# Performance work log

Hardware: AMD Instinct MI355X
Metric: run time of the kernel (lower is better)

## Reference

```python
import jax, jax.numpy as jnp
import numpy as np

# dims
B, S, H, D = 1, 2048, 32, 128
BLOCK = 64          # sparse_block_size
LOCAL = 16          # local_blocks
VERT = 8            # vert_stride
OFFSET = 0          # head_sliding_offset
SLIDE = max(1, VERT // H)  # head_sliding_step = max(1, int(vert_stride / num_heads))
NEG_INF = -1e30


def _sparse_mask():
    """Token-level local+vertical-stride causal mask, [H, S, S] bool."""
    pos = jnp.arange(S)
    blk = pos // BLOCK                                  # block index per token
    causal = pos[:, None] >= pos[None, :]               # [S, S]
    local = (blk[:, None] - blk[None, :]) < LOCAL       # [S, S]
    h = jnp.arange(H)
    # per-head vertical strips on key blocks
    vert = ((blk[None, None, :] + h[:, None, None] * SLIDE + OFFSET + 1) % VERT) == 0  # [H,1,S]
    return causal[None, :, :] & (local[None, :, :] | vert)  # [H, S, S]


def setup_inputs() -> dict:
    key = jax.random.key(0)
    kq, kk, kv = jax.random.split(key, 3)
    shape = (B, S, H, D)
    return {
        "query": jax.random.normal(kq, shape, dtype=jnp.float32),
        "key": jax.random.normal(kk, shape, dtype=jnp.float32),
        "value": jax.random.normal(kv, shape, dtype=jnp.float32),
    }


def reference(query, key, value):
    # inputs are bshd; sm_scale = head_dim**-0.5 (dkernel default)
    scale = 1.0 / jnp.sqrt(jnp.asarray(D, dtype=query.dtype))
    mask = _sparse_mask()                               # [H, S, S]
    scores = jnp.einsum("bqhd,bkhd->bhqk", query, key) * scale
    scores = jnp.where(mask[None], scores, NEG_INF)
    probs = jax.nn.softmax(scores, axis=-1)
    out = jnp.einsum("bhqk,bkhd->bqhd", probs, value)
    return out
```

## Files before the change

kernel.cpp:

```cpp
#include <hip/hip_runtime.h>


#define NH 32
#define HD 128
#define LOCALB 16

typedef __attribute__((ext_vector_type(8))) short short8;
typedef __attribute__((ext_vector_type(4))) float f32x4;

static __device__ __forceinline__ unsigned f2u(float f) {
    union { float f; unsigned u; } x; x.f = f; return x.u;
}
static __device__ __forceinline__ unsigned bfpk(float a, float b) {
    return ((f2u(a) + 0x8000u) >> 16) | ((f2u(b) + 0x8000u) & 0xFFFF0000u);
}
static __device__ __forceinline__ unsigned short f2bf(float f) {
    return (unsigned short)((f2u(f) + 0x8000u) >> 16);
}

static __device__ __forceinline__ void wg_barrier() {
    asm volatile("" ::: "memory");
    __builtin_amdgcn_s_waitcnt(0xC07F);
    __builtin_amdgcn_s_barrier();
    asm volatile("" ::: "memory");
}

static __device__ __forceinline__ bool blk_active(int qb, int kb, int h) {
    return ((qb - kb) < LOCALB) || (((kb + h + 1) & 7) == 0);
}

static __device__ __forceinline__ int krow(int kk) {
    return (kk & 3) | (((kk >> 2) & 1) << 4) | (((kk >> 3) & 3) << 2) | (kk & 32);
}

__global__ __launch_bounds__(256)
void sparse_attn_kernel(const float* __restrict__ Q,
                        const float* __restrict__ K,
                        const float* __restrict__ V,
                        float* __restrict__ O)
{
    const int id   = blockIdx.x;
    const int h    = (id & 7) * 4 + ((id >> 3) & 3);
    const int qb   = 31 - (id >> 5);

    const int tid  = threadIdx.x;
    const int wave = tid >> 6;
    const int lane = tid & 63;
    const int m16  = lane & 15;
    const int quad = lane >> 4;

    __shared__ __align__(16) char smem[64 * 136 * 2 + 128 * 36 * 4];
    unsigned short (*Ks)[136] = reinterpret_cast<unsigned short(*)[136]>(smem);
    unsigned (*Vp)[36] = reinterpret_cast<unsigned(*)[36]>(smem + 64 * 136 * 2);

    const float QSC = 0.08838834764831845f * 1.44269504088896f;
    short8 qf[4];
    {
        const int qrow = qb * 64 + wave * 16 + m16;
        const float* qp = Q + ((size_t)qrow * NH + h) * HD + quad * 8;
        #pragma unroll
        for (int ks = 0; ks < 4; ++ks) {
            const float4 a = *reinterpret_cast<const float4*>(qp + ks * 32);
            const float4 b = *reinterpret_cast<const float4*>(qp + ks * 32 + 4);
            short8 f;
            f[0]=(short)f2bf(a.x*QSC); f[1]=(short)f2bf(a.y*QSC);
            f[2]=(short)f2bf(a.z*QSC); f[3]=(short)f2bf(a.w*QSC);
            f[4]=(short)f2bf(b.x*QSC); f[5]=(short)f2bf(b.y*QSC);
            f[6]=(short)f2bf(b.z*QSC); f[7]=(short)f2bf(b.w*QSC);
            qf[ks] = f;
        }
    }

    f32x4 acc[8];
    #pragma unroll
    for (int dt = 0; dt < 8; ++dt) { acc[dt][0]=0.f; acc[dt][1]=0.f; acc[dt][2]=0.f; acc[dt][3]=0.f; }
    float mrow = -3.0e38f;
    float lrow = 0.f;

    const int kkey0 = tid >> 5;
    const int kd4   = (tid & 31) << 2;
    const int vkey0 = wave * 8 + (lane & 7);
    const int vd40  = (lane >> 3) << 2;
    const int vc    = wave * 4 + ((lane & 7) >> 1);

    int kb = 0;
    while (!blk_active(qb, kb, h)) ++kb;

    float4 kreg[8], vreg[8];
    {
        const float* kp = K + (size_t)kb * 262144 + (size_t)kkey0 * 4096 + h * 128 + kd4;
        #pragma unroll
        for (int it = 0; it < 8; ++it)
            kreg[it] = *reinterpret_cast<const float4*>(kp + it * 32768);
        const float* vp = V + (size_t)kb * 262144 + (size_t)vkey0 * 4096 + h * 128 + vd40;
        #pragma unroll
        for (int it = 0; it < 8; ++it)
            vreg[it] = *reinterpret_cast<const float4*>(vp + (it & 1) * 131072 + (it >> 1) * 32);
    }

    while (kb <= qb) {
        int nkb = kb + 1;
        while (nkb <= qb && !blk_active(qb, nkb, h)) ++nkb;

        wg_barrier();

        #pragma unroll
        for (int it = 0; it < 8; ++it) {
            const float4 kv = kreg[it];
            uint2 pk; pk.x = bfpk(kv.x, kv.y); pk.y = bfpk(kv.z, kv.w);
            *reinterpret_cast<uint2*>(&Ks[krow(it * 8 + kkey0)][kd4]) = pk;
        }
        if (nkb <= qb) {
            const float* kp = K + (size_t)nkb * 262144 + (size_t)kkey0 * 4096 + h * 128 + kd4;
            #pragma unroll
            for (int it = 0; it < 8; ++it)
                kreg[it] = *reinterpret_cast<const float4*>(kp + it * 32768);
        }

        #pragma unroll
        for (int it = 0; it < 8; ++it) {
            const int d4 = (it >> 1) * 32 + vd40;
            const float4 vv = vreg[it];
            const unsigned p0 = bfpk(vv.x, vv.y);
            const unsigned p1 = bfpk(vv.z, vv.w);
            const unsigned q0 = __shfl_xor(p0, 1);
            const unsigned q1 = __shfl_xor(p1, 1);
            const int c = (it & 1) * 16 + vc;
            if ((lane & 1) == 0) {
                Vp[d4 + 0][c] = (p0 & 0xFFFFu) | (q0 << 16);
                Vp[d4 + 1][c] = (p0 >> 16)     | (q0 & 0xFFFF0000u);
            } else {
                Vp[d4 + 2][c] = (q1 & 0xFFFFu) | (p1 << 16);
                Vp[d4 + 3][c] = (q1 >> 16)     | (p1 & 0xFFFF0000u);
            }
        }
        if (nkb <= qb) {
            const float* vp = V + (size_t)nkb * 262144 + (size_t)vkey0 * 4096 + h * 128 + vd40;
            #pragma unroll
            for (int it = 0; it < 8; ++it)
                vreg[it] = *reinterpret_cast<const float4*>(vp + (it & 1) * 131072 + (it >> 1) * 32);
        }

        wg_barrier();

        f32x4 sc[4];
        #pragma unroll
        for (int nt = 0; nt < 4; ++nt) {
            f32x4 s = {0.f, 0.f, 0.f, 0.f};
            #pragma unroll
            for (int ks = 0; ks < 4; ++ks) {
                const short8 a = *reinterpret_cast<const short8*>(&Ks[nt * 16 + m16][ks * 32 + quad * 8]);
                s = __builtin_amdgcn_mfma_f32_16x16x32_bf16(a, qf[ks], s, 0, 0, 0);
            }
            sc[nt] = s;
        }

        if (kb == qb) {
            const int qloc = wave * 16 + m16;
            #pragma unroll
            for (int nt = 0; nt < 4; ++nt) {
                const int kb0 = (nt >> 1) * 32 + quad * 8 + (nt & 1) * 4;
                #pragma unroll
                for (int r = 0; r < 4; ++r) {
                    if (kb0 + r > qloc) sc[nt][r] = -1.0e30f;
                }
            }
        }

        float mx = sc[0][0];
        #pragma unroll
        for (int nt = 0; nt < 4; ++nt) {
            #pragma unroll
            for (int r = 0; r < 4; ++r) mx = fmaxf(mx, sc[nt][r]);
        }
        mx = fmaxf(mx, __shfl_xor(mx, 16));
        mx = fmaxf(mx, __shfl_xor(mx, 32));
        const float mnew = fmaxf(mrow, mx);
        const float alpha = __builtin_exp2f(mrow - mnew);
        lrow *= alpha;
        #pragma unroll
        for (int dt = 0; dt < 8; ++dt) {
            acc[dt][0] *= alpha; acc[dt][1] *= alpha;
            acc[dt][2] *= alpha; acc[dt][3] *= alpha;
        }
        float rs = 0.f;
        #pragma unroll
        for (int nt = 0; nt < 4; ++nt) {
            #pragma unroll
            for (int r = 0; r < 4; ++r) {
                const float p = __builtin_exp2f(sc[nt][r] - mnew);
                sc[nt][r] = p;
                rs += p;
            }
        }
        rs += __shfl_xor(rs, 16);
        rs += __shfl_xor(rs, 32);
        lrow += rs;
        mrow = mnew;

        short8 pf[2];
        #pragma unroll
        for (int c = 0; c < 2; ++c) {
            union { unsigned u[4]; short8 s; } cv;
            cv.u[0] = bfpk(sc[2 * c][0],     sc[2 * c][1]);
            cv.u[1] = bfpk(sc[2 * c][2],     sc[2 * c][3]);
            cv.u[2] = bfpk(sc[2 * c + 1][0], sc[2 * c + 1][1]);
            cv.u[3] = bfpk(sc[2 * c + 1][2], sc[2 * c + 1][3]);
            pf[c] = cv.s;
        }

        #pragma unroll
        for (int dt = 0; dt < 8; ++dt) {
            #pragma unroll
            for (int c = 0; c < 2; ++c) {
                const short8 a = *reinterpret_cast<const short8*>(
                    &Vp[dt * 16 + m16][c * 16 + quad * 4]);
                acc[dt] = __builtin_amdgcn_mfma_f32_16x16x32_bf16(a, pf[c], acc[dt], 0, 0, 0);
            }
        }

        kb = nkb;
    }

    __syncthreads();
    float* Osf = reinterpret_cast<float*>(smem);
    {
        const float inv = 1.0f / lrow;
        const int q = wave * 16 + m16;
        #pragma unroll
        for (int dt = 0; dt < 8; ++dt) {
            f32x4 v = acc[dt];
            v[0] *= inv; v[1] *= inv; v[2] *= inv; v[3] *= inv;
            *reinterpret_cast<f32x4*>(&Osf[q * 132 + dt * 16 + quad * 4]) = v;
        }
    }
    __syncthreads();
    #pragma unroll
    for (int p = 0; p < 2; ++p) {
        const int row = p * 32 + (tid >> 3);
        const int dbase = (tid & 7) * 4;
        #pragma unroll
        for (int i = 0; i < 4; ++i) {
            const int d = i * 32 + dbase;
            const f32x4 v = *reinterpret_cast<const f32x4*>(&Osf[row * 132 + d]);
            *reinterpret_cast<f32x4*>(O + ((size_t)(qb * 64 + row) * NH + h) * HD + d) = v;
        }
    }
}

extern "C" void kernel_launch(void* const* d_in, const int* in_sizes, int n_in,
                              void* d_out, int out_size, void* d_ws, size_t ws_size,
                              hipStream_t stream) {
    const float* q = (const float*)d_in[0];
    const float* k = (const float*)d_in[1];
    const float* v = (const float*)d_in[2];
    float* out = (float*)d_out;
    sparse_attn_kernel<<<dim3(1024), dim3(256), 0, stream>>>(q, k, v, out);
}
```

Before: 208.1 us.

## Process two query blocks per workgroup to share K/V tile loads

Result: slower. 256.6 us (+23.3%).

```diff
diff --git a/kernel.cpp b/kernel.cpp
--- a/kernel.cpp
+++ b/kernel.cpp
@@ -3,7 +3,6 @@
 
 #define NH 32
 #define HD 128
-#define LOCALB 16
 
 typedef __attribute__((ext_vector_type(8))) short short8;
 typedef __attribute__((ext_vector_type(4))) float f32x4;
@@ -23,10 +22,6 @@
     __builtin_amdgcn_s_waitcnt(0xC07F);
     __builtin_amdgcn_s_barrier();
     asm volatile("" ::: "memory");
-}
-
-static __device__ __forceinline__ bool blk_active(int qb, int kb, int h) {
-    return ((qb - kb) < LOCALB) || (((kb + h + 1) & 7) == 0);
 }
 
 static __device__ __forceinline__ int krow(int kk) {
@@ -41,7 +36,9 @@
 {
     const int id   = blockIdx.x;
     const int h    = (id & 7) * 4 + ((id >> 3) & 3);
-    const int qb   = 31 - (id >> 5);
+    const int qmb  = 15 - (id >> 5);
+    const int qbA  = qmb * 2;
+    const int qbB  = qbA + 1;
 
     const int tid  = threadIdx.x;
     const int wave = tid >> 6;
@@ -54,9 +51,10 @@
     unsigned (*Vp)[36] = reinterpret_cast<unsigned(*)[36]>(smem + 64 * 136 * 2);
 
     const float QSC = 0.08838834764831845f * 1.44269504088896f;
-    short8 qf[4];
-    {
-        const int qrow = qb * 64 + wave * 16 + m16;
+    short8 qf[2][4];
+    #pragma unroll
+    for (int hx = 0; hx < 2; ++hx) {
+        const int qrow = qmb * 128 + hx * 64 + wave * 16 + m16;
         const float* qp = Q + ((size_t)qrow * NH + h) * HD + quad * 8;
         #pragma unroll
         for (int ks = 0; ks < 4; ++ks) {
@@ -67,54 +65,70 @@
             f[2]=(short)f2bf(a.z*QSC); f[3]=(short)f2bf(a.w*QSC);
             f[4]=(short)f2bf(b.x*QSC); f[5]=(short)f2bf(b.y*QSC);
             f[6]=(short)f2bf(b.z*QSC); f[7]=(short)f2bf(b.w*QSC);
-            qf[ks] = f;
-        }
-    }
-
-    f32x4 acc[8];
+            qf[hx][ks] = f;
+        }
+    }
+
+    f32x4 acc[2][8];
     #pragma unroll
-    for (int dt = 0; dt < 8; ++dt) { acc[dt][0]=0.f; acc[dt][1]=0.f; acc[dt][2]=0.f; acc[dt][3]=0.f; }
-    float mrow = -3.0e38f;
-    float lrow = 0.f;
-
-    const int kkey0 = tid >> 5;
-    const int kd4   = (tid & 31) << 2;
+    for (int hx = 0; hx < 2; ++hx)
+        #pragma unroll
+        for (int dt = 0; dt < 8; ++dt) {
+            acc[hx][dt][0]=0.f; acc[hx][dt][1]=0.f;
+            acc[hx][dt][2]=0.f; acc[hx][dt][3]=0.f;
+        }
+    float mrow[2] = { -3.0e38f, -3.0e38f };
+    float lrow[2] = { 0.f, 0.f };
+
+    const int kkey0 = tid >> 4;
+    const int kd8   = (tid & 15) << 3;
     const int vkey0 = wave * 8 + (lane & 7);
     const int vd40  = (lane >> 3) << 2;
     const int vc    = wave * 4 + ((lane & 7) >> 1);
 
+    const int lb = qbB - 16;
     int kb = 0;
-    while (!blk_active(qb, kb, h)) ++kb;
+    while (!((kb >= lb) || (((kb + h + 1) & 7) == 0))) ++kb;
 
     float4 kreg[8], vreg[8];
     {
-        const float* kp = K + (size_t)kb * 262144 + (size_t)kkey0 * 4096 + h * 128 + kd4;
-        #pragma unroll
-        for (int it = 0; it < 8; ++it)
-            kreg[it] = *reinterpret_cast<const float4*>(kp + it * 32768);
+        const float* kp = K + (size_t)kb * 262144 + (size_t)kkey0 * 4096 + h * 128 + kd8;
+        #pragma unroll
+        for (int it = 0; it < 4; ++it) {
+            kreg[2*it]   = *reinterpret_cast<const float4*>(kp + it * 65536);
+            kreg[2*it+1] = *reinterpret_cast<const float4*>(kp + it * 65536 + 4);
+        }
         const float* vp = V + (size_t)kb * 262144 + (size_t)vkey0 * 4096 + h * 128 + vd40;
         #pragma unroll
         for (int it = 0; it < 8; ++it)
             vreg[it] = *reinterpret_cast<const float4*>(vp + (it & 1) * 131072 + (it >> 1) * 32);
     }
 
-    while (kb <= qb) {
+    while (kb <= qbB) {
         int nkb = kb + 1;
-        while (nkb <= qb && !blk_active(qb, nkb, h)) ++nkb;
+        while (nkb <= qbB && !((nkb >= lb) || (((nkb + h + 1) & 7) == 0))) ++nkb;
+
+        const bool vert = ((kb + h + 1) & 7) == 0;
+        const bool actA = kb < qbB;
+        const bool actB = (kb >= qbB - 15) || vert;
 
         wg_barrier();
 
         #pragma unroll
-        for (int it = 0; it < 8; ++it) {
-            const float4 kv = kreg[it];
-            uint2 pk; pk.x = bfpk(kv.x, kv.y); pk.y = bfpk(kv.z, kv.w);
-            *reinterpret_cast<uint2*>(&Ks[krow(it * 8 + kkey0)][kd4]) = pk;
-        }
-        if (nkb <= qb) {
-            const float* kp = K + (size_t)nkb * 262144 + (size_t)kkey0 * 4096 + h * 128 + kd4;
-            #pragma unroll
-            for (int it = 0; it < 8; ++it)
-                kreg[it] = *reinterpret_cast<const float4*>(kp + it * 32768);
+        for (int it = 0; it < 4; ++it) {
+            const float4 a = kreg[2*it], b = kreg[2*it+1];
+            uint4 pk;
+            pk.x = bfpk(a.x, a.y); pk.y = bfpk(a.z, a.w);
+            pk.z = bfpk(b.x, b.y); pk.w = bfpk(b.z, b.w);
+            *reinterpret_cast<uint4*>(&Ks[krow(it * 16 + kkey0)][kd8]) = pk;
+        }
+        if (nkb <= qbB) {
+            const float* kp = K + (size_t)nkb * 262144 + (size_t)kkey0 * 4096 + h * 128 + kd8;
+            #pragma unroll
+            for (int it = 0; it < 4; ++it) {
+                kreg[2*it]   = *reinterpret_cast<const float4*>(kp + it * 65536);
+                kreg[2*it+1] = *reinterpret_cast<const float4*>(kp + it * 65536 + 4);
+            }
         }
 
         #pragma unroll
@@ -134,7 +148,7 @@
                 Vp[d4 + 3][c] = (q1 >> 16)     | (p1 & 0xFFFF0000u);
             }
         }
-        if (nkb <= qb) {
+        if (nkb <= qbB) {
             const float* vp = V + (size_t)nkb * 262144 + (size_t)vkey0 * 4096 + h * 128 + vd40;
             #pragma unroll
             for (int it = 0; it < 8; ++it)
@@ -143,70 +157,81 @@
 
         wg_barrier();
 
-        f32x4 sc[4];
+        f32x4 sc[2][4];
+        #pragma unroll
+        for (int hx = 0; hx < 2; ++hx)
+            #pragma unroll
+            for (int nt = 0; nt < 4; ++nt) {
+                sc[hx][nt][0]=0.f; sc[hx][nt][1]=0.f;
+                sc[hx][nt][2]=0.f; sc[hx][nt][3]=0.f;
+            }
         #pragma unroll
         for (int nt = 0; nt < 4; ++nt) {
-            f32x4 s = {0.f, 0.f, 0.f, 0.f};
             #pragma unroll
             for (int ks = 0; ks < 4; ++ks) {
                 const short8 a = *reinterpret_cast<const short8*>(&Ks[nt * 16 + m16][ks * 32 + quad * 8]);
-                s = __builtin_amdgcn_mfma_f32_16x16x32_bf16(a, qf[ks], s, 0, 0, 0);
-            }
-            sc[nt] = s;
-        }
-
-        if (kb == qb) {
-            const int qloc = wave * 16 + m16;
-            #pragma unroll
-            for (int nt = 0; nt < 4; ++nt) {
-                const int kb0 = (nt >> 1) * 32 + quad * 8 + (nt & 1) * 4;
+                if (actA) sc[0][nt] = __builtin_amdgcn_mfma_f32_16x16x32_bf16(a, qf[0][ks], sc[0][nt], 0, 0, 0);
+                if (actB) sc[1][nt] = __builtin_amdgcn_mfma_f32_16x16x32_bf16(a, qf[1][ks], sc[1][nt], 0, 0, 0);
+            }
+        }
+
+        #pragma unroll
+        for (int hx = 0; hx < 2; ++hx) {
+            if (kb == qbA + hx) {
+                const int qloc = wave * 16 + m16;
+                #pragma unroll
+                for (int nt = 0; nt < 4; ++nt) {
+                    const int kb0 = (nt >> 1) * 32 + quad * 8 + (nt & 1) * 4;
+                    #pragma unroll
+                    for (int r = 0; r < 4; ++r)
+                        if (kb0 + r > qloc) sc[hx][nt][r] = -1.0e30f;
+                }
+            }
+        }
+
+        short8 pf[2][2];
+        #pragma unroll
+        for (int hx = 0; hx < 2; ++hx) {
+            const bool act = hx ? actB : actA;
+            if (!act) continue;
+            float mx = sc[hx][0][0];
+            #pragma unroll
+            for (int nt = 0; nt < 4; ++nt)
+                #pragma unroll
+                for (int r = 0; r < 4; ++r) mx = fmaxf(mx, sc[hx][nt][r]);
+            mx = fmaxf(mx, __shfl_xor(mx, 16));
+            mx = fmaxf(mx, __shfl_xor(mx, 32));
+            const float mnew = fmaxf(mrow[hx], mx);
+            const float alpha = __builtin_exp2f(mrow[hx] - mnew);
+            lrow[hx] *= alpha;
+            #pragma unroll
+            for (int dt = 0; dt < 8; ++dt) {
+                acc[hx][dt][0] *= alpha; acc[hx][dt][1] *= alpha;
+                acc[hx][dt][2] *= alpha; acc[hx][dt][3] *= alpha;
+            }
+            float rs = 0.f;
+            #pragma unroll
+            for (int nt = 0; nt < 4; ++nt)
                 #pragma unroll
                 for (int r = 0; r < 4; ++r) {
-                    if (kb0 + r > qloc) sc[nt][r] = -1.0e30f;
+                    const float p = __builtin_exp2f(sc[hx][nt][r] - mnew);
+                    sc[hx][nt][r] = p;
+                    rs += p;
                 }
-            }
-        }
-
-        float mx = sc[0][0];
-        #pragma unroll
-        for (int nt = 0; nt < 4; ++nt) {
-            #pragma unroll
-            for (int r = 0; r < 4; ++r) mx = fmaxf(mx, sc[nt][r]);
-        }
-        mx = fmaxf(mx, __shfl_xor(mx, 16));
-        mx = fmaxf(mx, __shfl_xor(mx, 32));
-        const float mnew = fmaxf(mrow, mx);
-        const float alpha = __builtin_exp2f(mrow - mnew);
-        lrow *= alpha;
-        #pragma unroll
-        for (int dt = 0; dt < 8; ++dt) {
-            acc[dt][0] *= alpha; acc[dt][1] *= alpha;
-            acc[dt][2] *= alpha; acc[dt][3] *= alpha;
-        }
-        float rs = 0.f;
-        #pragma unroll
-        for (int nt = 0; nt < 4; ++nt) {
-            #pragma unroll
-            for (int r = 0; r < 4; ++r) {
-                const float p = __builtin_exp2f(sc[nt][r] - mnew);
-                sc[nt][r] = p;
-                rs += p;
-            }
-        }
-        rs += __shfl_xor(rs, 16);
-        rs += __shfl_xor(rs, 32);
-        lrow += rs;
-        mrow = mnew;
-
-        short8 pf[2];
-        #pragma unroll
-        for (int c = 0; c < 2; ++c) {
-            union { unsigned u[4]; short8 s; } cv;
-            cv.u[0] = bfpk(sc[2 * c][0],     sc[2 * c][1]);
-            cv.u[1] = bfpk(sc[2 * c][2],     sc[2 * c][3]);
-            cv.u[2] = bfpk(sc[2 * c + 1][0], sc[2 * c + 1][1]);
-            cv.u[3] = bfpk(sc[2 * c + 1][2], sc[2 * c + 1][3]);
-            pf[c] = cv.s;
+            rs += __shfl_xor(rs, 16);
+            rs += __shfl_xor(rs, 32);
+            lrow[hx] += rs;
+            mrow[hx] = mnew;
+
+            #pragma unroll
+            for (int c = 0; c < 2; ++c) {
+                union { unsigned u[4]; short8 s; } cv;
+                cv.u[0] = bfpk(sc[hx][2*c][0],   sc[hx][2*c][1]);
+                cv.u[1] = bfpk(sc[hx][2*c][2],   sc[hx][2*c][3]);
+                cv.u[2] = bfpk(sc[hx][2*c+1][0], sc[hx][2*c+1][1]);
+                cv.u[3] = bfpk(sc[hx][2*c+1][2], sc[hx][2*c+1][3]);
+                pf[hx][c] = cv.s;
+            }
         }
 
         #pragma unroll
@@ -215,35 +240,40 @@
             for (int c = 0; c < 2; ++c) {
                 const short8 a = *reinterpret_cast<const short8*>(
                     &Vp[dt * 16 + m16][c * 16 + quad * 4]);
-                acc[dt] = __builtin_amdgcn_mfma_f32_16x16x32_bf16(a, pf[c], acc[dt], 0, 0, 0);
+                if (actA) acc[0][dt] = __builtin_amdgcn_mfma_f32_16x16x32_bf16(a, pf[0][c], acc[0][dt], 0, 0, 0);
+                if (actB) acc[1][dt] = __builtin_amdgcn_mfma_f32_16x16x32_bf16(a, pf[1][c], acc[1][dt], 0, 0, 0);
             }
         }
 
         kb = nkb;
     }
 
-    __syncthreads();
     float* Osf = reinterpret_cast<float*>(smem);
-    {
-        const float inv = 1.0f / lrow;
-        const int q = wave * 16 + m16;
-        #pragma unroll
-        for (int dt = 0; dt < 8; ++dt) {
-            f32x4 v = acc[dt];
-            v[0] *= inv; v[1] *= inv; v[2] *= inv; v[3] *= inv;
-            *reinterpret_cast<f32x4*>(&Osf[q * 132 + dt * 16 + quad * 4]) = v;
-        }
-    }
-    __syncthreads();
     #pragma unroll
-    for (int p = 0; p < 2; ++p) {
-        const int row = p * 32 + (tid >> 3);
-        const int dbase = (tid & 7) * 4;
-        #pragma unroll
-        for (int i = 0; i < 4; ++i) {
-            const int d = i * 32 + dbase;
-            const f32x4 v = *reinterpret_cast<const f32x4*>(&Osf[row * 132 + d]);
-            *reinterpret_cast<f32x4*>(O + ((size_t)(qb * 64 + row) * NH + h) * HD + d) = v;
+    for (int hx = 0; hx < 2; ++hx) {
+        __syncthreads();
+        {
+            const float inv = 1.0f / lrow[hx];
+            const int q = wave * 16 + m16;
+            #pragma unroll
+            for (int dt = 0; dt < 8; ++dt) {
+                f32x4 v = acc[hx][dt];
+                v[0] *= inv; v[1] *= inv; v[2] *= inv; v[3] *= inv;
+                *reinterpret_cast<f32x4*>(&Osf[q * 132 + dt * 16 + quad * 4]) = v;
+            }
+        }
+        __syncthreads();
+        const int qbase = qmb * 128 + hx * 64;
+        #pragma unroll
+        for (int p = 0; p < 2; ++p) {
+            const int row = p * 32 + (tid >> 3);
+            const int dbase = (tid & 7) * 4;
+            #pragma unroll
+            for (int i = 0; i < 4; ++i) {
+                const int d = i * 32 + dbase;
+                const f32x4 v = *reinterpret_cast<const f32x4*>(&Osf[row * 132 + d]);
+                *reinterpret_cast<f32x4*>(O + ((size_t)(qbase + row) * NH + h) * HD + d) = v;
+            }
         }
     }
 }
@@ -255,5 +285,5 @@
     const float* k = (const float*)d_in[1];
     const float* v = (const float*)d_in[2];
     float* out = (float*)d_out;
-    sparse_attn_kernel<<<dim3(1024), dim3(256), 0, stream>>>(q, k, v, out);
-}
+    sparse_attn_kernel<<<dim3(512), dim3(256), 0, stream>>>(q, k, v, out);
+}
```
